# Kernel tuning notes

Measured on AMD Instinct MI355X. Metric: run time of the kernel, lower is better.

The kernel has to match this reference:

```python
import jax, jax.numpy as jnp
import numpy as np

B, H, W, D, K = 64, 32, 32, 128, 1024


def setup_inputs() -> dict:
    key = jax.random.key(0)
    k1, k2 = jax.random.split(key)
    z_e = jax.random.normal(k1, (B, H, W, D), dtype=jnp.float32)
    # GlorotUniform over (k, d): limit = sqrt(6 / (k + d))
    limit = float(np.sqrt(6.0 / (K + D)))
    codebook = jax.random.uniform(k2, (K, D), dtype=jnp.float32, minval=-limit, maxval=limit)
    return {"z_e": z_e, "codebook": codebook}


def reference(z_e, codebook):
    # Original: norm = ||z_e[..., None, :] - codebook||_2 over d, then argmin over k.
    # Squared distance has the same argmin; expand to avoid the (B,H,W,k,d) tensor:
    # ||z - c||^2 = ||z||^2 - 2 z.c + ||c||^2
    z2 = jnp.sum(z_e * z_e, axis=-1, keepdims=True)           # (B,H,W,1)
    c2 = jnp.sum(codebook * codebook, axis=-1)                # (k,)
    dots = jnp.einsum('bhwd,kd->bhwk', z_e, codebook)         # (B,H,W,k)
    dist2 = z2 - 2.0 * dots + c2                              # (B,H,W,k)
    q_z = jnp.argmin(dist2, axis=-1)                          # (B,H,W) int
    return q_z
```

## Files before the change

kernel.cpp:

```cpp
#include <hip/hip_runtime.h>
#include <stdint.h>

#define NPTS   65536
#define DDIM   128
#define KCODES 1024

typedef __attribute__((ext_vector_type(8))) _Float16  half8;
typedef __attribute__((ext_vector_type(4))) float     f32x4;
typedef __attribute__((ext_vector_type(4))) int       int4v;
typedef __attribute__((ext_vector_type(2))) _Float16  half2v;

__device__ __forceinline__ void split16(float x, _Float16& hi, _Float16& lo) {
  _Float16 h = (__builtin_fabsf(x) < 6.103515625e-05f) ? (_Float16)0.f : (_Float16)x;
  hi = h;
  lo = (_Float16)(__fmul_rn(__fsub_rn(x, (float)h), 2048.f));
}

__device__ __forceinline__ float np_sumsq_128(const float* __restrict__ row) {
  float r[8];
#pragma unroll
  for (int k = 0; k < 8; ++k) r[k] = __fmul_rn(row[k], row[k]);
  for (int i = 8; i < 128; i += 8)
#pragma unroll
    for (int k = 0; k < 8; ++k) r[k] = __fadd_rn(r[k], __fmul_rn(row[i + k], row[i + k]));
  float s01 = __fadd_rn(r[0], r[1]), s23 = __fadd_rn(r[2], r[3]);
  float s45 = __fadd_rn(r[4], r[5]), s67 = __fadd_rn(r[6], r[7]);
  return __fadd_rn(__fadd_rn(s01, s23), __fadd_rn(s45, s67));
}

__device__ __forceinline__ void async_copy16(const void* g, void* l) {
  auto gp = (const __attribute__((address_space(1))) unsigned int*)(uintptr_t)g;
  auto lp = (__attribute__((address_space(3))) unsigned int*)(unsigned)(uintptr_t)l;
  __builtin_amdgcn_global_load_lds(gp, lp, 16, 0, 0);
}

constexpr size_t SZ_B   = (size_t)KCODES * DDIM * 2;
constexpr size_t OFF_B1 = 0;
constexpr size_t OFF_B2 = SZ_B;
constexpr size_t OFF_C2 = 2 * SZ_B;
constexpr size_t WS_NEED = OFF_C2 + (size_t)KCODES * 4;

__global__ __launch_bounds__(256) void vq_prep_cb(const float* __restrict__ cb,
                                                  _Float16* __restrict__ B1,
                                                  _Float16* __restrict__ B2,
                                                  float* __restrict__ c2) {
  const int w = threadIdx.x >> 6, ln = threadIdx.x & 63;
  const int code = blockIdx.x * 4 + w;
  const float2 cv = ((const float2*)(cb + (size_t)code * DDIM))[ln];
  _Float16 h0, l0, h1, l1;
  split16(cv.x, h0, l0); split16(cv.y, h1, l1);
  const int kg = ln >> 2;
  const int o  = 2 * (ln & 3);
  const size_t dst = (size_t)code * DDIM + (size_t)((kg ^ (code & 15)) * 8 + o);
  *(half2v*)(B1 + dst) = (half2v){h0, h1};
  *(half2v*)(B2 + dst) = (half2v){l0, l1};

  if (threadIdx.x < 32) {
    const int cc = blockIdx.x * 4 + (threadIdx.x >> 3), jj = threadIdx.x & 7;
    const float* row = cb + (size_t)cc * DDIM;
    float e = row[jj];
    float acc = __fmul_rn(e, e);
    for (int i = 1; i < 16; ++i) {
      e = row[i * 8 + jj];
      acc = __fadd_rn(acc, __fmul_rn(e, e));
    }
    float a1 = __fadd_rn(acc, __shfl_xor(acc, 1));
    float a2 = __fadd_rn(a1, __shfl_xor(a1, 2));
    float a4 = __fadd_rn(a2, __shfl_xor(a2, 4));
    if (jj == 0) c2[cc] = a4;
  }
}

__global__ __launch_bounds__(256, 2) void vq_gemm(
    const float* __restrict__ z,
    const unsigned short* __restrict__ B1g, const unsigned short* __restrict__ B2g,
    const float* __restrict__ c2g, int* __restrict__ out) {
  __shared__ alignas(16) char smem[33792 + 4096 + 512];
  unsigned short* Bs1 = (unsigned short*)smem;
  unsigned short* Bs2 = (unsigned short*)(smem + 16384);
  float* c2sh = (float*)(smem + 33792);
  float* z2sh = (float*)(smem + 33792 + 4096);
  float* LsA  = (float*)smem;
  float* LsB  = (float*)(smem + 16896);

  const int tid = threadIdx.x;
  const int ln = tid & 63, wr = tid >> 6;
  const int l15 = ln & 15, q = ln >> 4;
  const size_t row0 = (size_t)blockIdx.x * 128;
  const float4* z4 = (const float4*)z;

  async_copy16(c2g + tid * 4, c2sh + tid * 4);

  auto stagez = [&](int cc, float* Ls) {
#pragma unroll
    for (int j = 0; j < 4; ++j) {
      const int idx = tid + j * 256;
      float4 v = z4[(row0 + cc * 32) * 32 + idx];
      *(float4*)&Ls[(idx >> 5) * 132 + (idx & 31) * 4] = v;
    }
  };
  stagez(0, LsA);
  for (int cc = 0; cc < 4; ++cc) {
    __syncthreads();
    if (cc < 3) stagez(cc + 1, (cc & 1) ? LsA : LsB);
    const float* Ls = (cc & 1) ? LsB : LsA;
    const int r = tid >> 3, jj = tid & 7;
    const float* row = &Ls[r * 132];
    float e = row[jj];
    float acc = __fmul_rn(e, e);
    for (int i = 1; i < 16; ++i) {
      e = row[i * 8 + jj];
      acc = __fadd_rn(acc, __fmul_rn(e, e));
    }
    float a1 = __fadd_rn(acc, __shfl_xor(acc, 1));
    float a2 = __fadd_rn(a1, __shfl_xor(a1, 2));
    float a4 = __fadd_rn(a2, __shfl_xor(a2, 4));
    if (jj == 0) z2sh[cc * 32 + r] = a4;
  }
  __syncthreads();

#pragma unroll
  for (int j = 0; j < 4; ++j) {
    const int s = tid + j * 256;
    async_copy16(B2g + s * 8, Bs2 + s * 8);
    async_copy16(B1g + s * 8, Bs1 + s * 8);
  }

  half8 a1f[2][4], a2f[2][4];
#pragma unroll
  for (int rf = 0; rf < 2; ++rf) {
    const float* zr = z + (row0 + wr * 32 + rf * 16 + l15) * DDIM;
#pragma unroll
    for (int ks = 0; ks < 4; ++ks) {
      float tmp[8];
      *(float4*)tmp       = *(const float4*)(zr + ks * 32 + q * 8);
      *(float4*)(tmp + 4) = *(const float4*)(zr + ks * 32 + q * 8 + 4);
      half8 h, l;
#pragma unroll
      for (int e = 0; e < 8; ++e) {
        _Float16 hh, ll;
        split16(tmp[e], hh, ll);
        h[e] = hh; l[e] = ll;
      }
      a1f[rf][ks] = h; a2f[rf][ks] = l;
    }
  }

  float mv[8];
  int mi[8];
#pragma unroll
  for (int i = 0; i < 8; ++i) { mv[i] = 3.0e38f; mi[i] = 0; }

  __syncthreads();

  float z2r[8];
#pragma unroll
  for (int rf = 0; rf < 2; ++rf)
#pragma unroll
    for (int reg = 0; reg < 4; ++reg)
      z2r[rf * 4 + reg] = z2sh[wr * 32 + rf * 16 + q * 4 + reg];

  for (int iter = 0; iter < 16; ++iter) {
    const int c0 = iter * 64;
    f32x4 acc[2][4];
#pragma unroll
    for (int rf = 0; rf < 2; ++rf)
#pragma unroll
      for (int cf = 0; cf < 4; ++cf) acc[rf][cf] = (f32x4){0.f, 0.f, 0.f, 0.f};

#pragma unroll
    for (int ks = 0; ks < 4; ++ks) {
      half8 b[4];
#pragma unroll
      for (int cf = 0; cf < 4; ++cf)
        b[cf] = *(const half8*)&Bs2[(cf * 16 + l15) * 128 + (((ks * 4 + q) ^ l15) * 8)];
#pragma unroll
      for (int rf = 0; rf < 2; ++rf)
#pragma unroll
        for (int cf = 0; cf < 4; ++cf)
          acc[rf][cf] = __builtin_amdgcn_mfma_f32_16x16x32_f16(a1f[rf][ks], b[cf],
                                                               acc[rf][cf], 0, 0, 0);
    }

    __syncthreads();
    if (iter < 15) {
#pragma unroll
      for (int j = 0; j < 4; ++j) {
        const int s = tid + j * 256;
        async_copy16(B2g + (size_t)(c0 + 64) * DDIM + s * 8, Bs2 + s * 8);
      }
    }

    half8 b1h[4][4];
#pragma unroll
    for (int ks = 0; ks < 4; ++ks) {
#pragma unroll
      for (int cf = 0; cf < 4; ++cf)
        b1h[ks][cf] =
            *(const half8*)&Bs1[(cf * 16 + l15) * 128 + (((ks * 4 + q) ^ l15) * 8)];
#pragma unroll
      for (int rf = 0; rf < 2; ++rf)
#pragma unroll
        for (int cf = 0; cf < 4; ++cf)
          acc[rf][cf] = __builtin_amdgcn_mfma_f32_16x16x32_f16(a2f[rf][ks], b1h[ks][cf],
                                                               acc[rf][cf], 0, 0, 0);
    }
#pragma unroll
    for (int rf = 0; rf < 2; ++rf)
#pragma unroll
      for (int cf = 0; cf < 4; ++cf) acc[rf][cf] = acc[rf][cf] * 4.8828125e-4f;

#pragma unroll
    for (int ks = 0; ks < 4; ++ks) {
#pragma unroll
      for (int rf = 0; rf < 2; ++rf)
#pragma unroll
        for (int cf = 0; cf < 4; ++cf)
          acc[rf][cf] = __builtin_amdgcn_mfma_f32_16x16x32_f16(a1f[rf][ks], b1h[ks][cf],
                                                               acc[rf][cf], 0, 0, 0);
    }

#pragma unroll
    for (int rf = 0; rf < 2; ++rf)
#pragma unroll
      for (int reg = 0; reg < 4; ++reg) {
        const int slot = rf * 4 + reg;
#pragma unroll
        for (int cf = 0; cf < 4; ++cf) {
          const float c2v = c2sh[c0 + cf * 16 + l15];
          float v = __fadd_rn(__builtin_fmaf(-2.f, acc[rf][cf][reg], z2r[slot]), c2v);
          int idx = c0 + cf * 16 + l15;
          if (v < mv[slot]) { mv[slot] = v; mi[slot] = idx; }
        }
      }

    __syncthreads();
    if (iter < 15) {
#pragma unroll
      for (int j = 0; j < 4; ++j) {
        const int s = tid + j * 256;
        async_copy16(B1g + (size_t)(c0 + 64) * DDIM + s * 8, Bs1 + s * 8);
      }
    }
  }

#pragma unroll
  for (int slot = 0; slot < 8; ++slot) {
    float v = mv[slot];
    int i = mi[slot];
#pragma unroll
    for (int m = 1; m <= 8; m <<= 1) {
      float ov = __shfl_xor(v, m);
      int oi = __shfl_xor(i, m);
      if (ov < v || (ov == v && oi < i)) { v = ov; i = oi; }
    }
    mv[slot] = v; mi[slot] = i;
  }

  if (l15 == 0) {
#pragma unroll
    for (int rf = 0; rf < 2; ++rf) {
      int4v r = {mi[rf * 4 + 0], mi[rf * 4 + 1], mi[rf * 4 + 2], mi[rf * 4 + 3]};
      *(int4v*)&out[row0 + wr * 32 + rf * 16 + q * 4] = r;
    }
  }
}

__global__ __launch_bounds__(256) void vq_fallback(const float* __restrict__ z,
                                                   const float* __restrict__ cb,
                                                   int* __restrict__ out) {
  __shared__ float zs[DDIM];
  __shared__ float z2s;
  __shared__ float bv[256];
  __shared__ int bi[256];
  const int p = blockIdx.x, tid = threadIdx.x;
  if (tid < DDIM) zs[tid] = z[(size_t)p * DDIM + tid];
  __syncthreads();
  if (tid == 0) z2s = np_sumsq_128(zs);
  __syncthreads();
  const float z2p = z2s;
  float best = 3.0e38f;
  int bidx = 0;
  for (int c = tid; c < KCODES; c += 256) {
    const float* cr = cb + (size_t)c * DDIM;
    double acc = 0.0;
#pragma unroll 8
    for (int d = 0; d < DDIM; ++d) acc += (double)zs[d] * (double)cr[d];
    float dfl = (float)acc;
    float c2k = np_sumsq_128(cr);
    float v = __fadd_rn(__fsub_rn(z2p, __fmul_rn(2.f, dfl)), c2k);
    if (v < best) { best = v; bidx = c; }
  }
  bv[tid] = best; bi[tid] = bidx;
  __syncthreads();
  for (int off = 128; off > 0; off >>= 1) {
    if (tid < off) {
      if (bv[tid + off] < bv[tid] || (bv[tid + off] == bv[tid] && bi[tid + off] < bi[tid])) {
        bv[tid] = bv[tid + off]; bi[tid] = bi[tid + off];
      }
    }
    __syncthreads();
  }
  if (tid == 0) out[p] = bi[0];
}

extern "C" void kernel_launch(void* const* d_in, const int* in_sizes, int n_in,
                              void* d_out, int out_size, void* d_ws, size_t ws_size,
                              hipStream_t stream) {
  (void)in_sizes; (void)n_in; (void)out_size;
  const float* z = (const float*)d_in[0];
  const float* cb = (const float*)d_in[1];
  int* out = (int*)d_out;

  if (d_ws != nullptr && ws_size >= WS_NEED) {
    char* ws = (char*)d_ws;
    _Float16* B1 = (_Float16*)(ws + OFF_B1);
    _Float16* B2 = (_Float16*)(ws + OFF_B2);
    float* c2 = (float*)(ws + OFF_C2);

    vq_prep_cb<<<KCODES / 4, 256, 0, stream>>>(cb, B1, B2, c2);
    vq_gemm<<<NPTS / 128, 256, 0, stream>>>(
        z, (const unsigned short*)(ws + OFF_B1), (const unsigned short*)(ws + OFF_B2),
        c2, out);
  } else {
    vq_fallback<<<NPTS, 256, 0, stream>>>(z, cb, out);
  }
}
```

Baseline: 120.4 us.

## Split codebook columns across warps, halve rows per block for higher occupancy

Each block now handles 64 points instead of 128, and the four waves are arranged 2x2 so each wave covers 32 rows and half of each 64-code tile. Per-wave accumulators and B fragments shrink, the launch-bounds hint rises to four blocks per CU, and the grid doubles. A shared-memory reduction merges the two column halves' argmin per row. The aim is more resident waves to hide LDS and memory latency, at the cost of reloading the codebook into LDS twice as often in total and re-reading B1 fragments.

After: 146.5 us. +21.7%, slower.

```diff
diff --git a/kernel.cpp b/kernel.cpp
--- a/kernel.cpp
+++ b/kernel.cpp
@@ -7,7 +7,6 @@
 
 typedef __attribute__((ext_vector_type(8))) _Float16  half8;
 typedef __attribute__((ext_vector_type(4))) float     f32x4;
-typedef __attribute__((ext_vector_type(4))) int       int4v;
 typedef __attribute__((ext_vector_type(2))) _Float16  half2v;
 
 __device__ __forceinline__ void split16(float x, _Float16& hi, _Float16& lo) {
@@ -71,22 +70,24 @@
   }
 }
 
-__global__ __launch_bounds__(256, 2) void vq_gemm(
+__global__ __launch_bounds__(256, 4) void vq_gemm(
     const float* __restrict__ z,
     const unsigned short* __restrict__ B1g, const unsigned short* __restrict__ B2g,
     const float* __restrict__ c2g, int* __restrict__ out) {
-  __shared__ alignas(16) char smem[33792 + 4096 + 512];
+  __shared__ alignas(16) char smem[38144];
   unsigned short* Bs1 = (unsigned short*)smem;
   unsigned short* Bs2 = (unsigned short*)(smem + 16384);
   float* c2sh = (float*)(smem + 33792);
-  float* z2sh = (float*)(smem + 33792 + 4096);
+  float* z2sh = (float*)(smem + 37888);
   float* LsA  = (float*)smem;
   float* LsB  = (float*)(smem + 16896);
 
   const int tid = threadIdx.x;
-  const int ln = tid & 63, wr = tid >> 6;
+  const int ln = tid & 63, w = tid >> 6;
+  const int wr = w >> 1, wc = w & 1;
   const int l15 = ln & 15, q = ln >> 4;
-  const size_t row0 = (size_t)blockIdx.x * 128;
+  const int wcb = wc * 32;
+  const size_t row0 = (size_t)blockIdx.x * 64;
   const float4* z4 = (const float4*)z;
 
   async_copy16(c2g + tid * 4, c2sh + tid * 4);
@@ -99,32 +100,26 @@
       *(float4*)&Ls[(idx >> 5) * 132 + (idx & 31) * 4] = v;
     }
   };
-  stagez(0, LsA);
-  for (int cc = 0; cc < 4; ++cc) {
-    __syncthreads();
-    if (cc < 3) stagez(cc + 1, (cc & 1) ? LsA : LsB);
-    const float* Ls = (cc & 1) ? LsB : LsA;
+  auto z2compute = [&](const float* Ls, int cc) {
     const int r = tid >> 3, jj = tid & 7;
-    const float* row = &Ls[r * 132];
-    float e = row[jj];
+    const float* rowp = &Ls[r * 132];
+    float e = rowp[jj];
     float acc = __fmul_rn(e, e);
     for (int i = 1; i < 16; ++i) {
-      e = row[i * 8 + jj];
+      e = rowp[i * 8 + jj];
       acc = __fadd_rn(acc, __fmul_rn(e, e));
     }
     float a1 = __fadd_rn(acc, __shfl_xor(acc, 1));
     float a2 = __fadd_rn(a1, __shfl_xor(a1, 2));
     float a4 = __fadd_rn(a2, __shfl_xor(a2, 4));
     if (jj == 0) z2sh[cc * 32 + r] = a4;
-  }
-  __syncthreads();
-
-#pragma unroll
-  for (int j = 0; j < 4; ++j) {
-    const int s = tid + j * 256;
-    async_copy16(B2g + s * 8, Bs2 + s * 8);
-    async_copy16(B1g + s * 8, Bs1 + s * 8);
-  }
+  };
+  stagez(0, LsA);
+  __syncthreads();
+  stagez(1, LsB);
+  z2compute(LsA, 0);
+  __syncthreads();
+  z2compute(LsB, 1);
 
   half8 a1f[2][4], a2f[2][4];
 #pragma unroll
@@ -146,6 +141,15 @@
     }
   }
 
+  __syncthreads();
+
+#pragma unroll
+  for (int j = 0; j < 4; ++j) {
+    const int s = tid + j * 256;
+    async_copy16(B2g + s * 8, Bs2 + s * 8);
+    async_copy16(B1g + s * 8, Bs1 + s * 8);
+  }
+
   float mv[8];
   int mi[8];
 #pragma unroll
@@ -153,31 +157,25 @@
 
   __syncthreads();
 
-  float z2r[8];
-#pragma unroll
-  for (int rf = 0; rf < 2; ++rf)
-#pragma unroll
-    for (int reg = 0; reg < 4; ++reg)
-      z2r[rf * 4 + reg] = z2sh[wr * 32 + rf * 16 + q * 4 + reg];
-
   for (int iter = 0; iter < 16; ++iter) {
     const int c0 = iter * 64;
-    f32x4 acc[2][4];
+    f32x4 acc[2][2];
 #pragma unroll
     for (int rf = 0; rf < 2; ++rf)
 #pragma unroll
-      for (int cf = 0; cf < 4; ++cf) acc[rf][cf] = (f32x4){0.f, 0.f, 0.f, 0.f};
+      for (int cf = 0; cf < 2; ++cf) acc[rf][cf] = (f32x4){0.f, 0.f, 0.f, 0.f};
 
 #pragma unroll
     for (int ks = 0; ks < 4; ++ks) {
-      half8 b[4];
-#pragma unroll
-      for (int cf = 0; cf < 4; ++cf)
-        b[cf] = *(const half8*)&Bs2[(cf * 16 + l15) * 128 + (((ks * 4 + q) ^ l15) * 8)];
+      half8 b[2];
+#pragma unroll
+      for (int cf = 0; cf < 2; ++cf)
+        b[cf] = *(const half8*)&Bs2[(wcb + cf * 16 + l15) * 128 +
+                                    (((ks * 4 + q) ^ l15) * 8)];
 #pragma unroll
       for (int rf = 0; rf < 2; ++rf)
 #pragma unroll
-        for (int cf = 0; cf < 4; ++cf)
+        for (int cf = 0; cf < 2; ++cf)
           acc[rf][cf] = __builtin_amdgcn_mfma_f32_16x16x32_f16(a1f[rf][ks], b[cf],
                                                                acc[rf][cf], 0, 0, 0);
     }
@@ -191,32 +189,37 @@
       }
     }
 
-    half8 b1h[4][4];
 #pragma unroll
     for (int ks = 0; ks < 4; ++ks) {
-#pragma unroll
-      for (int cf = 0; cf < 4; ++cf)
-        b1h[ks][cf] =
-            *(const half8*)&Bs1[(cf * 16 + l15) * 128 + (((ks * 4 + q) ^ l15) * 8)];
+      half8 b[2];
+#pragma unroll
+      for (int cf = 0; cf < 2; ++cf)
+        b[cf] = *(const half8*)&Bs1[(wcb + cf * 16 + l15) * 128 +
+                                    (((ks * 4 + q) ^ l15) * 8)];
 #pragma unroll
       for (int rf = 0; rf < 2; ++rf)
 #pragma unroll
-        for (int cf = 0; cf < 4; ++cf)
-          acc[rf][cf] = __builtin_amdgcn_mfma_f32_16x16x32_f16(a2f[rf][ks], b1h[ks][cf],
+        for (int cf = 0; cf < 2; ++cf)
+          acc[rf][cf] = __builtin_amdgcn_mfma_f32_16x16x32_f16(a2f[rf][ks], b[cf],
                                                                acc[rf][cf], 0, 0, 0);
     }
 #pragma unroll
     for (int rf = 0; rf < 2; ++rf)
 #pragma unroll
-      for (int cf = 0; cf < 4; ++cf) acc[rf][cf] = acc[rf][cf] * 4.8828125e-4f;
+      for (int cf = 0; cf < 2; ++cf) acc[rf][cf] = acc[rf][cf] * 4.8828125e-4f;
 
 #pragma unroll
     for (int ks = 0; ks < 4; ++ks) {
+      half8 b[2];
+#pragma unroll
+      for (int cf = 0; cf < 2; ++cf)
+        b[cf] = *(const half8*)&Bs1[(wcb + cf * 16 + l15) * 128 +
+                                    (((ks * 4 + q) ^ l15) * 8)];
 #pragma unroll
       for (int rf = 0; rf < 2; ++rf)
 #pragma unroll
-        for (int cf = 0; cf < 4; ++cf)
-          acc[rf][cf] = __builtin_amdgcn_mfma_f32_16x16x32_f16(a1f[rf][ks], b1h[ks][cf],
+        for (int cf = 0; cf < 2; ++cf)
+          acc[rf][cf] = __builtin_amdgcn_mfma_f32_16x16x32_f16(a1f[rf][ks], b[cf],
                                                                acc[rf][cf], 0, 0, 0);
     }
 
@@ -225,11 +228,12 @@
 #pragma unroll
       for (int reg = 0; reg < 4; ++reg) {
         const int slot = rf * 4 + reg;
-#pragma unroll
-        for (int cf = 0; cf < 4; ++cf) {
-          const float c2v = c2sh[c0 + cf * 16 + l15];
-          float v = __fadd_rn(__builtin_fmaf(-2.f, acc[rf][cf][reg], z2r[slot]), c2v);
-          int idx = c0 + cf * 16 + l15;
+        const float z2v = z2sh[wr * 32 + rf * 16 + q * 4 + reg];
+#pragma unroll
+        for (int cf = 0; cf < 2; ++cf) {
+          const float c2v = c2sh[c0 + wcb + cf * 16 + l15];
+          float v = __fadd_rn(__builtin_fmaf(-2.f, acc[rf][cf][reg], z2v), c2v);
+          int idx = c0 + wcb + cf * 16 + l15;
           if (v < mv[slot]) { mv[slot] = v; mi[slot] = idx; }
         }
       }
@@ -257,12 +261,24 @@
     mv[slot] = v; mi[slot] = i;
   }
 
+  float* rv = (float*)smem;
+  int* ri = (int*)(smem + 1024);
   if (l15 == 0) {
 #pragma unroll
-    for (int rf = 0; rf < 2; ++rf) {
-      int4v r = {mi[rf * 4 + 0], mi[rf * 4 + 1], mi[rf * 4 + 2], mi[rf * 4 + 3]};
-      *(int4v*)&out[row0 + wr * 32 + rf * 16 + q * 4] = r;
-    }
+    for (int rf = 0; rf < 2; ++rf)
+#pragma unroll
+      for (int reg = 0; reg < 4; ++reg) {
+        const int row = wr * 32 + rf * 16 + q * 4 + reg;
+        rv[row * 2 + wc] = mv[rf * 4 + reg];
+        ri[row * 2 + wc] = mi[rf * 4 + reg];
+      }
+  }
+  __syncthreads();
+  if (tid < 64) {
+    float v0 = rv[tid * 2 + 0], v1 = rv[tid * 2 + 1];
+    int i0 = ri[tid * 2 + 0], i1 = ri[tid * 2 + 1];
+    int i = (v1 < v0 || (v1 == v0 && i1 < i0)) ? i1 : i0;
+    out[row0 + tid] = i;
   }
 }
 
@@ -319,7 +335,7 @@
     float* c2 = (float*)(ws + OFF_C2);
 
     vq_prep_cb<<<KCODES / 4, 256, 0, stream>>>(cb, B1, B2, c2);
-    vq_gemm<<<NPTS / 128, 256, 0, stream>>>(
+    vq_gemm<<<NPTS / 64, 256, 0, stream>>>(
         z, (const unsigned short*)(ws + OFF_B1), (const unsigned short*)(ws + OFF_B2),
         c2, out);
   } else {
```
